# Optimization experiments

Measured on AMD Instinct MI355X. Metric: run time of the kernel, lower is better.

The kernel has to match this reference:

```python
import jax, jax.numpy as jnp
import numpy as np

ABS_DIM, HIDDEN, ACTION_DIM, N_TASKS, B = 512, 512, 18, 16, 8192
W_SCALE = 0.001


def setup_inputs() -> dict:
    key = jax.random.key(0)
    k1, k2, k3, k4, k5 = jax.random.split(key, 5)
    x = jax.random.normal(k1, (B, ABS_DIM), dtype=jnp.float32)
    task_id = jax.random.randint(k2, (B,), 0, N_TASKS)
    action = jax.random.randint(k3, (B,), 0, ACTION_DIM)
    # Per-task weight banks (MultiLinear), w_scale=0.001
    W1 = jax.random.normal(k4, (N_TASKS, ABS_DIM, HIDDEN), dtype=jnp.float32) * W_SCALE
    b1 = jnp.zeros((N_TASKS, HIDDEN), dtype=jnp.float32)
    W2 = jax.random.normal(k5, (N_TASKS, HIDDEN, ACTION_DIM), dtype=jnp.float32) * W_SCALE
    b2 = jnp.zeros((N_TASKS, ACTION_DIM), dtype=jnp.float32)
    return {"x": x, "task_id": task_id, "action": action,
            "W1": W1, "b1": b1, "W2": W2, "b2": b2}


def _multi_linear(x, W, b, task_id):
    # x: [B, din], W: [T, din, dout], b: [T, dout]
    # Compute all experts then select per-sample (dense grouped-GEMM form).
    y_all = jnp.einsum('bi,tio->tbo', x, W) + b[:, None, :]  # [T, B, dout]
    rows = jnp.arange(x.shape[0])
    return y_all[task_id, rows]  # [B, dout]


def reference(x, task_id, action, W1, b1, W2, b2):
    h = jax.nn.relu(_multi_linear(x, W1, b1, task_id))          # [B, H]
    logits = _multi_linear(h, W2, b2, task_id)                  # [B, A]
    logprobs = jax.nn.log_softmax(logits, axis=1)               # [B, A]
    rows = jnp.arange(x.shape[0])
    log_pi_a = logprobs[rows, action][:, None]                  # [B, 1]
    ent = -jnp.sum(jnp.exp(logprobs) * logprobs, axis=1, keepdims=True)  # [B, 1]
    # forward output: concat of log_pi_a and entropy (action passes through)
    return jnp.concatenate([log_pi_a, ent], axis=1)             # [B, 2]
```

## Files before the change

### kernel.cpp

```cpp
#include <hip/hip_runtime.h>
#include <hip/hip_bf16.h>

#define B_N   8192
#define DIN   512
#define DH    512
#define NACT  18
#define NTASK 16
#define BM    64
#define GBN   128
#define BK    64
#define PJ    20
#define NSLOT 640

typedef __attribute__((ext_vector_type(8))) short  short8v;
typedef __attribute__((ext_vector_type(8))) unsigned short ushort8v;
typedef __attribute__((ext_vector_type(4))) unsigned short ushort4v;
typedef __attribute__((ext_vector_type(4))) float  float4v;
typedef __attribute__((ext_vector_type(2))) float  float2v;

typedef const __attribute__((address_space(1))) void* gas_ptr;
typedef __attribute__((address_space(3))) void* las_ptr;

__device__ __forceinline__ unsigned short f2bf(float f) {
  union { float f; unsigned int u; } c; c.f = f;
  unsigned int u = c.u;
  u += 0x7fffu + ((u >> 16) & 1u);
  return (unsigned short)(u >> 16);
}

__global__ __launch_bounds__(256) void k_prep(
    const float* __restrict__ W1, const float* __restrict__ W2,
    const int* __restrict__ task_id,
    short* __restrict__ W1T, short* __restrict__ W2T,
    int* __restrict__ tbl, int* __restrict__ rowidx) {
  __shared__ __align__(16) char ldsT[64 * 144];
  __shared__ float ldsB[64 * 19];
  __shared__ int c4[4][NTASK], cur4[4][NTASK];
  int bx = blockIdx.x, tid = threadIdx.x;

  if (bx == 0) {
    if (tid < 64) ((int*)c4)[tid] = 0;
    __syncthreads();
    for (int i = tid; i < B_N; i += 256)
      atomicAdd(&c4[i >> 11][task_id[i]], 1);
    __syncthreads();
    if (tid == 0) {
      int acc = 0;
#pragma unroll
      for (int t = 0; t < NTASK; ++t) {
        int c = c4[0][t] + c4[1][t] + c4[2][t] + c4[3][t];
        tbl[t] = c; tbl[16 + t] = acc;
        int o = acc;
#pragma unroll
        for (int q = 0; q < 4; ++q) { cur4[q][t] = o; o += c4[q][t]; }
        acc += c;
      }
    }
    __syncthreads();
    for (int i = tid; i < B_N; i += 256) {
      int t = task_id[i];
      rowidx[atomicAdd(&cur4[i >> 11][t], 1)] = i;
    }
  } else if (bx <= 1024) {
    int r = bx & 7;
    int q = ((bx - r) >> 3) - (r == 0 ? 1 : 0);
    int t = r + ((q >> 6) << 3);
    int sub = q & 63;
    int kb = sub >> 3, nb = sub & 7;

    int nc4 = tid & 15, kr4 = tid >> 4;
    const float* src = W1 + ((size_t)t * DIN + (size_t)(kb * 64 + kr4 * 4)) * DH
                          + nb * 64 + nc4 * 4;
    float4v r0 = *(const float4v*)(src);
    float4v r1 = *(const float4v*)(src + DH);
    float4v r2 = *(const float4v*)(src + 2 * DH);
    float4v r3 = *(const float4v*)(src + 3 * DH);
#pragma unroll
    for (int i = 0; i < 4; ++i) {
      int n = nc4 * 4 + i;
      ushort4v pk;
      pk[0] = f2bf(r0[i]); pk[1] = f2bf(r1[i]);
      pk[2] = f2bf(r2[i]); pk[3] = f2bf(r3[i]);
      int c = (kr4 >> 1) ^ ((n >> 2) & 7);
      *(ushort4v*)(ldsT + n * 144 + c * 16 + (kr4 & 1) * 8) = pk;
    }
    __syncthreads();
    int n = tid >> 2, k16 = (tid & 3) << 4;
    int c0 = k16 >> 3;
    int f  = (n >> 2) & 7;
    ushort8v v0 = *(ushort8v*)(ldsT + n * 144 + ((c0 ^ f) * 16));
    ushort8v v1 = *(ushort8v*)(ldsT + n * 144 + (((c0 + 1) ^ f) * 16));
    short* dst = W1T + ((size_t)t * DH + nb * 64 + n) * DIN + kb * 64 + k16;
    *(ushort8v*)dst       = v0;
    *(ushort8v*)(dst + 8) = v1;
  } else {
    int u = bx - 1025;
    int t = u >> 3, k0 = (u & 7) * 64;
    for (int i = tid; i < 64 * NACT; i += 256) {
      int kk = i / NACT, j = i - kk * NACT;
      ldsB[kk * 19 + j] = W2[((size_t)t * DIN + k0 + kk) * NACT + j];
    }
    __syncthreads();
    for (int o = tid; o < 32 * 64; o += 256) {
      int j = o >> 6, kk = o & 63;
      float val = (j < NACT) ? ldsB[kk * 19 + j] : 0.0f;
      W2T[((size_t)t * 32 + j) * DIN + k0 + kk] = (short)f2bf(val);
    }
  }
}

__global__ __launch_bounds__(256, 3) void k_gemm1(
    const float* __restrict__ x, const float* __restrict__ bias1,
    const short* __restrict__ W1T, const short* __restrict__ W2Tg,
    const int* __restrict__ tbl, const int* __restrict__ rowidx,
    float* __restrict__ pbuf) {
  __shared__ __align__(16) short sA[2][BM * 72];
  __shared__ __align__(16) short sB[2][GBN * BK];
  short* sH = sB[0];
  __shared__ int s_rows[64];
  int tid = threadIdx.x, lane = tid & 63, wave = tid >> 6;

  int b = blockIdx.x;
  int t = -1, rel = 0;
  if (b < NSLOT) {
    int r = b & 7, q = b >> 3;
    int n0t = (tbl[r] + 63) >> 6, n1t = (tbl[r + 8] + 63) >> 6;
    if (q < 4 * n0t) { t = r; rel = q; }
    else if (q < 4 * (n0t + n1t)) { t = r + 8; rel = q - 4 * n0t; }
    else return;
  } else {
    int j = b - NSLOT;
    for (int r = 0; r < 8; ++r) {
      int n0t = (tbl[r] + 63) >> 6, n1t = (tbl[r + 8] + 63) >> 6;
      int P = 4 * (n0t + n1t);
      int S = (P > 80) ? (P - 80) : 0;
      if (j < S) {
        int q = 80 + j;
        if (q < 4 * n0t) { t = r; rel = q; }
        else { t = r + 8; rel = q - 4 * n0t; }
        break;
      }
      j -= S;
    }
    if (t < 0) return;
  }
  int itile = rel >> 2, cs = rel & 3;
  int cnt_t = tbl[t], off_t = tbl[16 + t];
  int row0 = off_t + itile * 64;
  int mcnt = cnt_t - itile * 64; if (mcnt > 64) mcnt = 64;
  int n0 = cs * GBN;
  int wm = wave >> 1, wn = wave & 1;

  if (tid < 64) {
    int idx = row0 + tid;
    if (idx > B_N - 1) idx = B_N - 1;
    s_rows[tid] = rowidx[idx];
  }
  __syncthreads();

  short8v w2r[2][4];
#pragma unroll
  for (int fn = 0; fn < 2; ++fn) {
    int j = fn * 16 + (lane & 15);
    const short* wr = W2Tg + ((size_t)t * 32 + j) * DIN + n0 + ((lane >> 4) << 3);
#pragma unroll
    for (int ks = 0; ks < 4; ++ks)
      w2r[fn][ks] = *(const short8v*)(wr + ks * 32);
  }

  int arow = tid >> 2, akc = (tid & 3) << 4;
  const float* xrow = x + (size_t)s_rows[arow] * DIN + akc;
  const short* Bbase = W1T + ((size_t)t * DH + n0) * DIN;

  float4v La0, La1, La2, La3;
#define LOAD_A(k0e) {                                                        \
    const float* xs_ = xrow + (k0e);                                         \
    La0 = *(const float4v*)xs_;                                              \
    La1 = *(const float4v*)(xs_ + 4);                                        \
    La2 = *(const float4v*)(xs_ + 8);                                        \
    La3 = *(const float4v*)(xs_ + 12); }
#define WRITE_A(buf) {                                                       \
    ushort8v p0, p1;                                                         \
    _Pragma("unroll") for (int i_ = 0; i_ < 4; ++i_) {                       \
      p0[i_] = f2bf(La0[i_]); p0[4 + i_] = f2bf(La1[i_]);                    \
      p1[i_] = f2bf(La2[i_]); p1[4 + i_] = f2bf(La3[i_]); }                  \
    *(ushort8v*)&sA[buf][arow * 72 + akc] = p0;                              \
    *(ushort8v*)&sA[buf][arow * 72 + akc + 8] = p1; }
#define STAGE_B(buf, k0e)                                                    \
  _Pragma("unroll") for (int it = 0; it < 4; ++it) {                         \
    int ch = it * 256 + tid; int row = ch >> 3, cc = ch & 7;                 \
    int sc = cc ^ (row & 7);                                                 \
    __builtin_amdgcn_global_load_lds(                                        \
        (gas_ptr)(const void*)(Bbase + (size_t)row * DIN + (k0e) + sc * 8),  \
        (las_ptr)(void*)(&sB[buf][ch * 8]), 16, 0, 0);                       \
  }

  LOAD_A(0)
  STAGE_B(0, 0)
  WRITE_A(0)
  asm volatile("s_waitcnt vmcnt(0)" ::: "memory");
  __syncthreads();

  float4v acc[2][4];
#pragma unroll
  for (int i = 0; i < 2; ++i)
#pragma unroll
    for (int j = 0; j < 4; ++j) acc[i][j] = (float4v)0.0f;

#pragma unroll
  for (int step = 0; step < 8; ++step) {
    const int p = step & 1;
    if (step < 7) {
      LOAD_A((step + 1) * BK)
      STAGE_B(p ^ 1, (step + 1) * BK)
    }
#pragma unroll
    for (int ks = 0; ks < 2; ++ks) {
      short8v a[2], bfr[4];
#pragma unroll
      for (int fm = 0; fm < 2; ++fm) {
        int r = wm * 32 + fm * 16 + (lane & 15);
        int c = ks * 4 + (lane >> 4);
        a[fm] = *(const short8v*)&sA[p][r * 72 + c * 8];
      }
#pragma unroll
      for (int fn = 0; fn < 4; ++fn) {
        int r = wn * 64 + fn * 16 + (lane & 15);
        int c = (ks * 4 + (lane >> 4)) ^ (r & 7);
        bfr[fn] = *(const short8v*)&sB[p][r * BK + c * 8];
      }
#pragma unroll
      for (int fm = 0; fm < 2; ++fm)
#pragma unroll
        for (int fn = 0; fn < 4; ++fn)
          acc[fm][fn] = __builtin_amdgcn_mfma_f32_16x16x32_bf16(a[fm], bfr[fn], acc[fm][fn], 0, 0, 0);
    }
    if (step < 7) {
      WRITE_A(p ^ 1)
    }
    asm volatile("s_waitcnt vmcnt(0)" ::: "memory");
    __syncthreads();
  }

  float bias[4];
#pragma unroll
  for (int fn = 0; fn < 4; ++fn)
    bias[fn] = bias1[t * DH + n0 + wn * 64 + fn * 16 + (lane & 15)];
#pragma unroll
  for (int fn = 0; fn < 4; ++fn) {
    int n = wn * 64 + fn * 16 + (lane & 15);
#pragma unroll
    for (int fm = 0; fm < 2; ++fm) {
#pragma unroll
      for (int r = 0; r < 4; ++r) {
        int m = wm * 32 + fm * 16 + ((lane >> 4) << 2) + r;
        float v = fmaxf(acc[fm][fn][r] + bias[fn], 0.0f);
        *(short*)((char*)sH + m * 256 + (((n >> 3) ^ (m & 7)) << 4) + ((n & 7) << 1)) =
            (short)f2bf(v);
      }
    }
  }
  __syncthreads();

  float4v acc2[2];
  acc2[0] = (float4v)0.0f; acc2[1] = (float4v)0.0f;
#pragma unroll
  for (int ks = 0; ks < 4; ++ks) {
    int mrow = wave * 16 + (lane & 15);
    int ca = (ks * 4 + (lane >> 4)) ^ (mrow & 7);
    short8v af = *(const short8v*)((char*)sH + mrow * 256 + (ca << 4));
#pragma unroll
    for (int fn = 0; fn < 2; ++fn)
      acc2[fn] = __builtin_amdgcn_mfma_f32_16x16x32_bf16(af, w2r[fn][ks], acc2[fn], 0, 0, 0);
  }
#pragma unroll
  for (int fn = 0; fn < 2; ++fn) {
#pragma unroll
    for (int r = 0; r < 4; ++r) {
      int m = wave * 16 + ((lane >> 4) << 2) + r;
      int j = fn * 16 + (lane & 15);
      if (m < mcnt && j < PJ)
        pbuf[((size_t)cs * B_N + row0 + m) * PJ + j] = acc2[fn][r];
    }
  }
#undef STAGE_B
#undef LOAD_A
#undef WRITE_A
}

__global__ __launch_bounds__(256) void k_soft(
    const float* __restrict__ pbuf, const float* __restrict__ bias2,
    const int* __restrict__ task_id, const int* __restrict__ action,
    const int* __restrict__ rowidx, float* __restrict__ out) {
  __shared__ float acc[256 * PJ];
  int tid = threadIdx.x;
  int base = blockIdx.x * 256;
#pragma unroll
  for (int it = 0; it < 5; ++it) {
    int idx = it * 256 + tid;
    int row = idx / 5, j4 = idx - row * 5;
    float4v s = (float4v)0.0f;
#pragma unroll
    for (int c = 0; c < 4; ++c)
      s += *(const float4v*)&pbuf[((size_t)c * B_N + base + row) * PJ + j4 * 4];
    *(float4v*)&acc[row * PJ + j4 * 4] = s;
  }
  __syncthreads();

  int srow = base + tid;
  int orig = rowidx[srow];
  int t = task_id[orig], act = action[orig];
  float lg[NACT];
#pragma unroll
  for (int j = 0; j < NACT; ++j) lg[j] = acc[tid * PJ + j] + bias2[t * NACT + j];
  float mx = lg[0];
#pragma unroll
  for (int j = 1; j < NACT; ++j) mx = fmaxf(mx, lg[j]);
  float s1 = 0.0f, s2 = 0.0f, la = 0.0f;
#pragma unroll
  for (int j = 0; j < NACT; ++j) {
    float e = __expf(lg[j] - mx);
    s1 += e; s2 += e * lg[j];
    la = (j == act) ? lg[j] : la;
  }
  float logZ = __logf(s1);
  float2v o;
  o[0] = la - mx - logZ;
  o[1] = (mx + logZ) - s2 / s1;
  *(float2v*)(out + (size_t)orig * 2) = o;
}

extern "C" void kernel_launch(void* const* d_in, const int* in_sizes, int n_in,
                              void* d_out, int out_size, void* d_ws, size_t ws_size,
                              hipStream_t stream) {
  const float* x       = (const float*)d_in[0];
  const int*   task_id = (const int*)d_in[1];
  const int*   action  = (const int*)d_in[2];
  const float* W1      = (const float*)d_in[3];
  const float* b1      = (const float*)d_in[4];
  const float* W2      = (const float*)d_in[5];
  const float* b2      = (const float*)d_in[6];
  float* out = (float*)d_out;

  char* ws = (char*)d_ws;
  int* tbl    = (int*)ws;
  int* rowidx = (int*)(ws + 4096);
  size_t off = 36864;
  short* W1T  = (short*)(ws + off);  off += (size_t)NTASK * DH * DIN * 2;
  short* W2T  = (short*)(ws + off);  off += (size_t)NTASK * 32 * DIN * 2;
  float* pbuf = (float*)(ws + off);

  k_prep<<<1153, 256, 0, stream>>>(W1, W2, task_id, W1T, W2T, tbl, rowidx);
  k_gemm1<<<NSLOT + 576, 256, 0, stream>>>(x, b1, W1T, W2T, tbl, rowidx, pbuf);
  k_soft<<<32, 256, 0, stream>>>(pbuf, b2, task_id, action, rowidx, out);
}
```

Measured before the change: 44.50 us.

## Shrink GEMM1 tiles to 64x64x32 and split hidden into eight slices

The fused first GEMM now uses a 64x64 output tile with BK=32 instead of 64x128 with BK=64. The hidden dimension is split into 8 column slices instead of 4, and each wave computes 16 rows across all 64 columns. LDS use shrinks, occupancy hint rises to 5 blocks per CU, and the W2 slice is staged through LDS rather than held in registers. The grid roughly doubles to raise parallelism and occupancy. In exchange, x is re-read and re-converted twice as often, the K loop has twice as many barrier steps, and the softmax kernel must reduce 8 partial sums instead of 4.

```diff
diff --git a/kernel.cpp b/kernel.cpp
--- a/kernel.cpp
+++ b/kernel.cpp
@@ -7,10 +7,11 @@
 #define NACT  18
 #define NTASK 16
 #define BM    64
-#define GBN   128
-#define BK    64
+#define BN    64
+#define BK    32
 #define PJ    20
-#define NSLOT 640
+#define NSLOT 1280
+#define SPILL 256
 
 typedef __attribute__((ext_vector_type(8))) short  short8v;
 typedef __attribute__((ext_vector_type(8))) unsigned short ushort8v;
@@ -67,7 +68,6 @@
     int t = r + ((q >> 6) << 3);
     int sub = q & 63;
     int kb = sub >> 3, nb = sub & 7;
-
     int nc4 = tid & 15, kr4 = tid >> 4;
     const float* src = W1 + ((size_t)t * DIN + (size_t)(kb * 64 + kr4 * 4)) * DH
                           + nb * 64 + nc4 * 4;
@@ -109,14 +109,15 @@
   }
 }
 
-__global__ __launch_bounds__(256, 3) void k_gemm1(
+__global__ __launch_bounds__(256, 5) void k_gemm1(
     const float* __restrict__ x, const float* __restrict__ bias1,
     const short* __restrict__ W1T, const short* __restrict__ W2Tg,
     const int* __restrict__ tbl, const int* __restrict__ rowidx,
     float* __restrict__ pbuf) {
-  __shared__ __align__(16) short sA[2][BM * 72];
-  __shared__ __align__(16) short sB[2][GBN * BK];
-  short* sH = sB[0];
+  __shared__ __align__(16) short sA[2][BM * 40];
+  __shared__ __align__(16) short sB[2][BN * BK];
+  short* sH  = sA[0];
+  short* sW2 = sB[0];
   __shared__ int s_rows[64];
   int tid = threadIdx.x, lane = tid & 63, wave = tid >> 6;
 
@@ -125,31 +126,30 @@
   if (b < NSLOT) {
     int r = b & 7, q = b >> 3;
     int n0t = (tbl[r] + 63) >> 6, n1t = (tbl[r + 8] + 63) >> 6;
-    if (q < 4 * n0t) { t = r; rel = q; }
-    else if (q < 4 * (n0t + n1t)) { t = r + 8; rel = q - 4 * n0t; }
+    if (q < 8 * n0t) { t = r; rel = q; }
+    else if (q < 8 * (n0t + n1t)) { t = r + 8; rel = q - 8 * n0t; }
     else return;
   } else {
     int j = b - NSLOT;
     for (int r = 0; r < 8; ++r) {
       int n0t = (tbl[r] + 63) >> 6, n1t = (tbl[r + 8] + 63) >> 6;
-      int P = 4 * (n0t + n1t);
-      int S = (P > 80) ? (P - 80) : 0;
+      int P = 8 * (n0t + n1t);
+      int S = (P > 160) ? (P - 160) : 0;
       if (j < S) {
-        int q = 80 + j;
-        if (q < 4 * n0t) { t = r; rel = q; }
-        else { t = r + 8; rel = q - 4 * n0t; }
+        int q = 160 + j;
+        if (q < 8 * n0t) { t = r; rel = q; }
+        else { t = r + 8; rel = q - 8 * n0t; }
         break;
       }
       j -= S;
     }
     if (t < 0) return;
   }
-  int itile = rel >> 2, cs = rel & 3;
+  int itile = rel >> 3, cs = rel & 7;
   int cnt_t = tbl[t], off_t = tbl[16 + t];
   int row0 = off_t + itile * 64;
   int mcnt = cnt_t - itile * 64; if (mcnt > 64) mcnt = 64;
-  int n0 = cs * GBN;
-  int wm = wave >> 1, wn = wave & 1;
+  int n0 = cs * BN;
 
   if (tid < 64) {
     int idx = row0 + tid;
@@ -158,42 +158,26 @@
   }
   __syncthreads();
 
-  short8v w2r[2][4];
-#pragma unroll
-  for (int fn = 0; fn < 2; ++fn) {
-    int j = fn * 16 + (lane & 15);
-    const short* wr = W2Tg + ((size_t)t * 32 + j) * DIN + n0 + ((lane >> 4) << 3);
-#pragma unroll
-    for (int ks = 0; ks < 4; ++ks)
-      w2r[fn][ks] = *(const short8v*)(wr + ks * 32);
-  }
-
-  int arow = tid >> 2, akc = (tid & 3) << 4;
-  const float* xrow = x + (size_t)s_rows[arow] * DIN + akc;
+  int arow = tid >> 2, ak8 = (tid & 3) << 3;
+  const float* xrow = x + (size_t)s_rows[arow] * DIN + ak8;
   const short* Bbase = W1T + ((size_t)t * DH + n0) * DIN;
-
-  float4v La0, La1, La2, La3;
+  int brow = tid >> 2, bc = tid & 3;
+  int bsc = bc ^ ((brow >> 1) & 3);
+
+  float4v La0, La1;
 #define LOAD_A(k0e) {                                                        \
     const float* xs_ = xrow + (k0e);                                         \
     La0 = *(const float4v*)xs_;                                              \
-    La1 = *(const float4v*)(xs_ + 4);                                        \
-    La2 = *(const float4v*)(xs_ + 8);                                        \
-    La3 = *(const float4v*)(xs_ + 12); }
+    La1 = *(const float4v*)(xs_ + 4); }
 #define WRITE_A(buf) {                                                       \
-    ushort8v p0, p1;                                                         \
+    ushort8v p0;                                                             \
     _Pragma("unroll") for (int i_ = 0; i_ < 4; ++i_) {                       \
-      p0[i_] = f2bf(La0[i_]); p0[4 + i_] = f2bf(La1[i_]);                    \
-      p1[i_] = f2bf(La2[i_]); p1[4 + i_] = f2bf(La3[i_]); }                  \
-    *(ushort8v*)&sA[buf][arow * 72 + akc] = p0;                              \
-    *(ushort8v*)&sA[buf][arow * 72 + akc + 8] = p1; }
+      p0[i_] = f2bf(La0[i_]); p0[4 + i_] = f2bf(La1[i_]); }                  \
+    *(ushort8v*)&sA[buf][arow * 40 + ak8] = p0; }
 #define STAGE_B(buf, k0e)                                                    \
-  _Pragma("unroll") for (int it = 0; it < 4; ++it) {                         \
-    int ch = it * 256 + tid; int row = ch >> 3, cc = ch & 7;                 \
-    int sc = cc ^ (row & 7);                                                 \
     __builtin_amdgcn_global_load_lds(                                        \
-        (gas_ptr)(const void*)(Bbase + (size_t)row * DIN + (k0e) + sc * 8),  \
-        (las_ptr)(void*)(&sB[buf][ch * 8]), 16, 0, 0);                       \
-  }
+        (gas_ptr)(const void*)(Bbase + (size_t)brow * DIN + (k0e) + bsc * 8),\
+        (las_ptr)(void*)(&sB[buf][tid * 8]), 16, 0, 0);
 
   LOAD_A(0)
   STAGE_B(0, 0)
@@ -201,77 +185,71 @@
   asm volatile("s_waitcnt vmcnt(0)" ::: "memory");
   __syncthreads();
 
-  float4v acc[2][4];
-#pragma unroll
-  for (int i = 0; i < 2; ++i)
-#pragma unroll
-    for (int j = 0; j < 4; ++j) acc[i][j] = (float4v)0.0f;
-
-#pragma unroll
-  for (int step = 0; step < 8; ++step) {
+  float4v acc[4];
+#pragma unroll
+  for (int i = 0; i < 4; ++i) acc[i] = (float4v)0.0f;
+
+#pragma unroll
+  for (int step = 0; step < 16; ++step) {
     const int p = step & 1;
-    if (step < 7) {
+    if (step < 15) {
       LOAD_A((step + 1) * BK)
       STAGE_B(p ^ 1, (step + 1) * BK)
     }
-#pragma unroll
-    for (int ks = 0; ks < 2; ++ks) {
-      short8v a[2], bfr[4];
-#pragma unroll
-      for (int fm = 0; fm < 2; ++fm) {
-        int r = wm * 32 + fm * 16 + (lane & 15);
-        int c = ks * 4 + (lane >> 4);
-        a[fm] = *(const short8v*)&sA[p][r * 72 + c * 8];
-      }
-#pragma unroll
-      for (int fn = 0; fn < 4; ++fn) {
-        int r = wn * 64 + fn * 16 + (lane & 15);
-        int c = (ks * 4 + (lane >> 4)) ^ (r & 7);
-        bfr[fn] = *(const short8v*)&sB[p][r * BK + c * 8];
-      }
-#pragma unroll
-      for (int fm = 0; fm < 2; ++fm)
-#pragma unroll
-        for (int fn = 0; fn < 4; ++fn)
-          acc[fm][fn] = __builtin_amdgcn_mfma_f32_16x16x32_bf16(a[fm], bfr[fn], acc[fm][fn], 0, 0, 0);
-    }
-    if (step < 7) {
+    short8v a, bfr[4];
+    {
+      int r = wave * 16 + (lane & 15);
+      a = *(const short8v*)&sA[p][r * 40 + ((lane >> 4) << 3)];
+    }
+#pragma unroll
+    for (int fn = 0; fn < 4; ++fn) {
+      int r = fn * 16 + (lane & 15);
+      int c = (lane >> 4) ^ ((r >> 1) & 3);
+      bfr[fn] = *(const short8v*)&sB[p][r * BK + c * 8];
+    }
+#pragma unroll
+    for (int fn = 0; fn < 4; ++fn)
+      acc[fn] = __builtin_amdgcn_mfma_f32_16x16x32_bf16(a, bfr[fn], acc[fn], 0, 0, 0);
+    if (step < 15) {
       WRITE_A(p ^ 1)
     }
     asm volatile("s_waitcnt vmcnt(0)" ::: "memory");
     __syncthreads();
   }
 
-  float bias[4];
-#pragma unroll
-  for (int fn = 0; fn < 4; ++fn)
-    bias[fn] = bias1[t * DH + n0 + wn * 64 + fn * 16 + (lane & 15)];
 #pragma unroll
   for (int fn = 0; fn < 4; ++fn) {
-    int n = wn * 64 + fn * 16 + (lane & 15);
-#pragma unroll
-    for (int fm = 0; fm < 2; ++fm) {
-#pragma unroll
-      for (int r = 0; r < 4; ++r) {
-        int m = wm * 32 + fm * 16 + ((lane >> 4) << 2) + r;
-        float v = fmaxf(acc[fm][fn][r] + bias[fn], 0.0f);
-        *(short*)((char*)sH + m * 256 + (((n >> 3) ^ (m & 7)) << 4) + ((n & 7) << 1)) =
-            (short)f2bf(v);
-      }
-    }
+    int n = fn * 16 + (lane & 15);
+    float bias = bias1[t * DH + n0 + n];
+#pragma unroll
+    for (int r = 0; r < 4; ++r) {
+      int m = wave * 16 + ((lane >> 4) << 2) + r;
+      float v = fmaxf(acc[fn][r] + bias, 0.0f);
+      *(short*)((char*)sH + m * 128 + (((n >> 3) ^ (m & 7)) << 4) + ((n & 7) << 1)) =
+          (short)f2bf(v);
+    }
+  }
+  {
+    int j = tid >> 3, c2 = tid & 7;
+    ushort8v w = *(const ushort8v*)(W2Tg + ((size_t)t * 32 + j) * DIN + n0 + c2 * 8);
+    *(ushort8v*)&sW2[(j * 8 + (c2 ^ (j & 7))) * 8] = w;
   }
   __syncthreads();
 
   float4v acc2[2];
   acc2[0] = (float4v)0.0f; acc2[1] = (float4v)0.0f;
 #pragma unroll
-  for (int ks = 0; ks < 4; ++ks) {
+  for (int ks = 0; ks < 2; ++ks) {
     int mrow = wave * 16 + (lane & 15);
     int ca = (ks * 4 + (lane >> 4)) ^ (mrow & 7);
-    short8v af = *(const short8v*)((char*)sH + mrow * 256 + (ca << 4));
-#pragma unroll
-    for (int fn = 0; fn < 2; ++fn)
-      acc2[fn] = __builtin_amdgcn_mfma_f32_16x16x32_bf16(af, w2r[fn][ks], acc2[fn], 0, 0, 0);
+    short8v af = *(const short8v*)((char*)sH + mrow * 128 + (ca << 4));
+#pragma unroll
+    for (int fn = 0; fn < 2; ++fn) {
+      int j = fn * 16 + (lane & 15);
+      int cb = (ks * 4 + (lane >> 4)) ^ (j & 7);
+      short8v bf = *(const short8v*)&sW2[(j * 8 + cb) * 8];
+      acc2[fn] = __builtin_amdgcn_mfma_f32_16x16x32_bf16(af, bf, acc2[fn], 0, 0, 0);
+    }
   }
 #pragma unroll
   for (int fn = 0; fn < 2; ++fn) {
@@ -301,7 +279,7 @@
     int row = idx / 5, j4 = idx - row * 5;
     float4v s = (float4v)0.0f;
 #pragma unroll
-    for (int c = 0; c < 4; ++c)
+    for (int c = 0; c < 8; ++c)
       s += *(const float4v*)&pbuf[((size_t)c * B_N + base + row) * PJ + j4 * 4];
     *(float4v*)&acc[row * PJ + j4 * 4] = s;
   }
@@ -351,6 +329,6 @@
   float* pbuf = (float*)(ws + off);
 
   k_prep<<<1153, 256, 0, stream>>>(W1, W2, task_id, W1T, W2T, tbl, rowidx);
-  k_gemm1<<<NSLOT + 576, 256, 0, stream>>>(x, b1, W1T, W2T, tbl, rowidx, pbuf);
+  k_gemm1<<<NSLOT + SPILL, 256, 0, stream>>>(x, b1, W1T, W2T, tbl, rowidx, pbuf);
   k_soft<<<32, 256, 0, stream>>>(pbuf, b2, task_id, action, rowidx, out);
 }
```

Result: faster. 43.54 us (-2.2%).
